# Kernel optimization log

Measured on AMD Instinct MI355X. Metric: run time of the kernel, lower is better.

## Reference

```python
import jax, jax.numpy as jnp
import numpy as np

N_ROIS = 8192
C, S = 256, 7
D = C * S * S  # 12544 flattened RoI feature dim
NUM_CLASSES = 31
DIMS = {"cls": NUM_CLASSES + 1, "reg": 4 * NUM_CLASSES, "face": 3, "colour": 7, "motion": 2}


def setup_inputs() -> dict:
    key = jax.random.key(0)
    ks = jax.random.split(key, 6)
    x = jax.random.normal(ks[0], (N_ROIS, C, S, S), dtype=jnp.float32)
    inp = {"x": x}
    for i, (name, out_dim) in enumerate(DIMS.items()):
        inp[f"W_{name}"] = 0.01 * jax.random.normal(ks[i + 1], (D, out_dim), dtype=jnp.float32)
        inp[f"b_{name}"] = jnp.zeros((out_dim,), dtype=jnp.float32)
    return inp


def reference(x, W_cls, b_cls, W_reg, b_reg, W_face, b_face,
              W_colour, b_colour, W_motion, b_motion):
    # AttributeBBoxHead.forward with with_avg_pool=False: flatten then 5 linear heads.
    xf = x.reshape(x.shape[0], -1)  # (N, 12544)
    cls_score = xf @ W_cls + b_cls        # (N, 32)
    bbox_pred = xf @ W_reg + b_reg        # (N, 124)
    face_score = xf @ W_face + b_face     # (N, 3)
    colour_score = xf @ W_colour + b_colour  # (N, 7)
    motion_score = xf @ W_motion + b_motion  # (N, 2)
    return (cls_score, bbox_pred, face_score, colour_score, motion_score)
```

## Files before the change

kernel.cpp:

```cpp
#include <hip/hip_runtime.h>
#include <hip/hip_bf16.h>
#include <stdint.h>

#define D_DIM 12544
#define NROIS 8192
#define NCOLS 168
#define NCPAD 176
#define NT 11
#define SPLIT 8
#define KSPLIT (D_DIM / SPLIT)
#define BK 32
#define KITERS (KSPLIT / BK)
#define BM 64

#define XROW_B 72
#define WCOL_B 80
#define WL_COLS 192
#define XL_BYTES (BM * XROW_B)
#define WL_BYTES (WL_COLS * WCOL_B)
#define BUF_BYTES (XL_BYTES + WL_BYTES)

typedef __attribute__((ext_vector_type(8))) short short8;
typedef __attribute__((ext_vector_type(4))) float floatx4;

__device__ __forceinline__ uint32_t pk_bf16(float a, float b) {
    uint32_t ua = __float_as_uint(a);
    uint32_t ub = __float_as_uint(b);
    ua = (ua + 0x7FFFu + ((ua >> 16) & 1u)) >> 16;
    ub = (ub + 0x7FFFu + ((ub >> 16) & 1u)) >> 16;
    return ua | (ub << 16);
}

__global__ __launch_bounds__(256) void pack_w(
        const float* __restrict__ Wc, const float* __restrict__ Wr,
        const float* __restrict__ Wf, const float* __restrict__ Wco,
        const float* __restrict__ Wm, uint16_t* __restrict__ Wp) {
    __shared__ float tile[64][33];
    int k0 = blockIdx.x * 64;
    int c0 = blockIdx.y * 32;
    int t  = threadIdx.x;

    int rc = t & 31;
    int rk = t >> 5;
#pragma unroll
    for (int rr = 0; rr < 8; ++rr) {
        int k = rr * 8 + rk;
        int kk = k0 + k;
        int c = c0 + rc;
        float v = 0.f;
        if (c < 32)       v = Wc[(size_t)kk * 32  + c];
        else if (c < 156) v = Wr[(size_t)kk * 124 + (c - 32)];
        else if (c < 159) v = Wf[(size_t)kk * 3   + (c - 156)];
        else if (c < 166) v = Wco[(size_t)kk * 7  + (c - 159)];
        else if (c < 168) v = Wm[(size_t)kk * 2   + (c - 166)];
        tile[k][rc] = v;
    }
    __syncthreads();

    int wc = t >> 3;
    int wk = t & 7;
    int c  = c0 + wc;
    if (c < NCPAD) {
        uint32_t o[4];
#pragma unroll
        for (int j = 0; j < 4; ++j)
            o[j] = pk_bf16(tile[wk * 8 + 2 * j][wc], tile[wk * 8 + 2 * j + 1][wc]);
        uint4 v = make_uint4(o[0], o[1], o[2], o[3]);
        *(uint4*)(Wp + (size_t)c * D_DIM + k0 + wk * 8) = v;
    }
}

__global__ __launch_bounds__(256) void gemm_split(const float* __restrict__ X,
                                                  const uint16_t* __restrict__ Wp,
                                                  uint16_t* __restrict__ parts) {
    __shared__ __attribute__((aligned(16))) char lds[2 * BUF_BYTES];

    int b     = blockIdx.x;
    int split = b & 7;
    int rb    = b >> 3;
    int row0  = rb * BM;
    int kbase = split * KSPLIT;

    int t    = threadIdx.x;
    int wave = t >> 6;
    int lane = t & 63;

    int sx_row = t >> 2;
    int sx_kc  = t & 3;
    const float* xg = X + (size_t)(row0 + sx_row) * D_DIM + kbase + sx_kc * 8;

    int sw_col = t >> 2;
    int sw_ch  = t & 3;
    int c0g = sw_col       < NCPAD ? sw_col       : NCPAD - 1;
    int c1g = sw_col + 64  < NCPAD ? sw_col + 64  : NCPAD - 1;
    int c2g = sw_col + 128 < NCPAD ? sw_col + 128 : NCPAD - 1;
    const uint16_t* wg0 = Wp + (size_t)c0g * D_DIM + kbase + sw_ch * 8;
    const uint16_t* wg1 = Wp + (size_t)c1g * D_DIM + kbase + sw_ch * 8;
    const uint16_t* wg2 = Wp + (size_t)c2g * D_DIM + kbase + sw_ch * 8;

    int x_st = sx_row * XROW_B + sx_kc * 16;
    int w_st0 = XL_BYTES + (sw_col)       * WCOL_B + sw_ch * 16;
    int w_st1 = XL_BYTES + (sw_col + 64)  * WCOL_B + sw_ch * 16;
    int w_st2 = XL_BYTES + (sw_col + 128) * WCOL_B + sw_ch * 16;

    int n    = lane & 15;
    int quad = lane >> 4;
    int xf_off = (wave * 16 + n) * XROW_B + quad * 16;
    int wf_off = XL_BYTES + n * WCOL_B + quad * 16;

    floatx4 acc[NT];
#pragma unroll
    for (int tt = 0; tt < NT; ++tt) acc[tt] = (floatx4)0.f;

    float4 px0 = *(const float4*)xg;
    float4 px1 = *(const float4*)(xg + 4);
    xg += BK;
    short8 pw0 = *(const short8*)wg0; wg0 += BK;
    short8 pw1 = *(const short8*)wg1; wg1 += BK;
    short8 pw2 = *(const short8*)wg2; wg2 += BK;
    {
        union { uint32_t u[4]; short8 s; } p;
        p.u[0] = pk_bf16(px0.x, px0.y); p.u[1] = pk_bf16(px0.z, px0.w);
        p.u[2] = pk_bf16(px1.x, px1.y); p.u[3] = pk_bf16(px1.z, px1.w);
        *(short8*)(lds + x_st) = p.s;
        *(short8*)(lds + w_st0) = pw0;
        *(short8*)(lds + w_st1) = pw1;
        *(short8*)(lds + w_st2) = pw2;
    }
    int cur = 0;

    for (int it = 0; it < KITERS; ++it) {
        __syncthreads();

        float4 nx0, nx1; short8 nw0, nw1, nw2;
        bool more = (it + 1 < KITERS);
        if (more) {
            nx0 = *(const float4*)xg;
            nx1 = *(const float4*)(xg + 4);
            xg += BK;
            nw0 = *(const short8*)wg0; wg0 += BK;
            nw1 = *(const short8*)wg1; wg1 += BK;
            nw2 = *(const short8*)wg2; wg2 += BK;
        }

        const char* cb = lds + cur * BUF_BYTES;
        short8 xf = *(const short8*)(cb + xf_off);
#pragma unroll
        for (int tt = 0; tt < NT; ++tt) {
            short8 wf = *(const short8*)(cb + wf_off + tt * (16 * WCOL_B));
            acc[tt] = __builtin_amdgcn_mfma_f32_16x16x32_bf16(wf, xf, acc[tt], 0, 0, 0);
        }

        if (more) {
            char* nb = lds + (cur ^ 1) * BUF_BYTES;
            union { uint32_t u[4]; short8 s; } p;
            p.u[0] = pk_bf16(nx0.x, nx0.y); p.u[1] = pk_bf16(nx0.z, nx0.w);
            p.u[2] = pk_bf16(nx1.x, nx1.y); p.u[3] = pk_bf16(nx1.z, nx1.w);
            *(short8*)(nb + x_st) = p.s;
            *(short8*)(nb + w_st0) = nw0;
            *(short8*)(nb + w_st1) = nw1;
            *(short8*)(nb + w_st2) = nw2;
            cur ^= 1;
        }
    }

    uint16_t* pb = parts + ((size_t)split * NROIS + row0 + wave * 16 + n) * NCOLS;
#pragma unroll
    for (int tt = 0; tt < NT; ++tt) {
        int col0 = tt * 16 + quad * 4;
        if (col0 + 3 < NCOLS) {
            uint32_t lo = pk_bf16(acc[tt].x, acc[tt].y);
            uint32_t hi = pk_bf16(acc[tt].z, acc[tt].w);
            uint2 v = make_uint2(lo, hi);
            *(uint2*)(pb + col0) = v;
        }
    }
}

__global__ void reduce_out(const uint16_t* __restrict__ parts,
                           const float* __restrict__ bc, const float* __restrict__ br,
                           const float* __restrict__ bf, const float* __restrict__ bco,
                           const float* __restrict__ bm, float* __restrict__ out) {
    int r = blockIdx.x;
    int c = threadIdx.x;
    if (c >= NCOLS) return;
    const size_t S = (size_t)NROIS * NCOLS;
    size_t off = (size_t)r * NCOLS + c;
    float v = 0.f;
#pragma unroll
    for (int s = 0; s < SPLIT; ++s)
        v += __uint_as_float((uint32_t)parts[off + (size_t)s * S] << 16);
    float bias; size_t oidx;
    if (c < 32)       { bias = bc[c];        oidx = (size_t)r * 32  + c; }
    else if (c < 156) { bias = br[c - 32];   oidx = 262144u  + (size_t)r * 124 + (c - 32); }
    else if (c < 159) { bias = bf[c - 156];  oidx = 1277952u + (size_t)r * 3   + (c - 156); }
    else if (c < 166) { bias = bco[c - 159]; oidx = 1302528u + (size_t)r * 7   + (c - 159); }
    else              { bias = bm[c - 166];  oidx = 1359872u + (size_t)r * 2   + (c - 166); }
    out[oidx] = v + bias;
}

extern "C" void kernel_launch(void* const* d_in, const int* in_sizes, int n_in,
                              void* d_out, int out_size, void* d_ws, size_t ws_size,
                              hipStream_t stream) {
    const float* X   = (const float*)d_in[0];
    const float* Wc  = (const float*)d_in[1];
    const float* bc  = (const float*)d_in[2];
    const float* Wr  = (const float*)d_in[3];
    const float* br  = (const float*)d_in[4];
    const float* Wf  = (const float*)d_in[5];
    const float* bfa = (const float*)d_in[6];
    const float* Wco = (const float*)d_in[7];
    const float* bco = (const float*)d_in[8];
    const float* Wm  = (const float*)d_in[9];
    const float* bm  = (const float*)d_in[10];

    uint16_t* Wp    = (uint16_t*)d_ws;
    uint16_t* parts = (uint16_t*)((char*)d_ws + (size_t)NCPAD * D_DIM * 2);
    float* out = (float*)d_out;

    pack_w<<<dim3(D_DIM / 64, 6), 256, 0, stream>>>(Wc, Wr, Wf, Wco, Wm, Wp);
    gemm_split<<<1024, 256, 0, stream>>>(X, Wp, parts);
    reduce_out<<<NROIS, 192, 0, stream>>>(parts, bc, br, bfa, bco, bm, out);
}
```

Before: 609.3 us.

## Deepen global prefetch to two stages with ping-pong registers in split GEMM

The K loop of the split-K GEMM now holds two sets of prefetch registers (A/B) and unrolls by two. Global loads are issued two iterations ahead instead of one, while LDS stays double-buffered. This gives more memory latency hiding for the streamed X reads. The launch bounds also now request 4 blocks per CU, which caps registers. The extra prefetch registers could cause spills or lower occupancy under that cap.

Result: no change. 620.0 us (+1.8%).

```diff
diff --git a/kernel.cpp b/kernel.cpp
--- a/kernel.cpp
+++ b/kernel.cpp
@@ -70,9 +70,9 @@
     }
 }
 
-__global__ __launch_bounds__(256) void gemm_split(const float* __restrict__ X,
-                                                  const uint16_t* __restrict__ Wp,
-                                                  uint16_t* __restrict__ parts) {
+__global__ __launch_bounds__(256, 4) void gemm_split(const float* __restrict__ X,
+                                                     const uint16_t* __restrict__ Wp,
+                                                     uint16_t* __restrict__ parts) {
     __shared__ __attribute__((aligned(16))) char lds[2 * BUF_BYTES];
 
     int b     = blockIdx.x;
@@ -98,7 +98,7 @@
     const uint16_t* wg1 = Wp + (size_t)c1g * D_DIM + kbase + sw_ch * 8;
     const uint16_t* wg2 = Wp + (size_t)c2g * D_DIM + kbase + sw_ch * 8;
 
-    int x_st = sx_row * XROW_B + sx_kc * 16;
+    int x_st  = sx_row * XROW_B + sx_kc * 16;
     int w_st0 = XL_BYTES + (sw_col)       * WCOL_B + sw_ch * 16;
     int w_st1 = XL_BYTES + (sw_col + 64)  * WCOL_B + sw_ch * 16;
     int w_st2 = XL_BYTES + (sw_col + 128) * WCOL_B + sw_ch * 16;
@@ -112,55 +112,63 @@
 #pragma unroll
     for (int tt = 0; tt < NT; ++tt) acc[tt] = (floatx4)0.f;
 
-    float4 px0 = *(const float4*)xg;
-    float4 px1 = *(const float4*)(xg + 4);
-    xg += BK;
-    short8 pw0 = *(const short8*)wg0; wg0 += BK;
-    short8 pw1 = *(const short8*)wg1; wg1 += BK;
-    short8 pw2 = *(const short8*)wg2; wg2 += BK;
-    {
+    float4 ax0, ax1; short8 aw0, aw1, aw2;
+    float4 bx0, bx1; short8 bw0, bw1, bw2;
+
+    auto issueA = [&]() {
+        ax0 = *(const float4*)xg; ax1 = *(const float4*)(xg + 4); xg += BK;
+        aw0 = *(const short8*)wg0; wg0 += BK;
+        aw1 = *(const short8*)wg1; wg1 += BK;
+        aw2 = *(const short8*)wg2; wg2 += BK;
+    };
+    auto issueB = [&]() {
+        bx0 = *(const float4*)xg; bx1 = *(const float4*)(xg + 4); xg += BK;
+        bw0 = *(const short8*)wg0; wg0 += BK;
+        bw1 = *(const short8*)wg1; wg1 += BK;
+        bw2 = *(const short8*)wg2; wg2 += BK;
+    };
+    auto stageA = [&](char* nb) {
         union { uint32_t u[4]; short8 s; } p;
-        p.u[0] = pk_bf16(px0.x, px0.y); p.u[1] = pk_bf16(px0.z, px0.w);
-        p.u[2] = pk_bf16(px1.x, px1.y); p.u[3] = pk_bf16(px1.z, px1.w);
-        *(short8*)(lds + x_st) = p.s;
-        *(short8*)(lds + w_st0) = pw0;
-        *(short8*)(lds + w_st1) = pw1;
-        *(short8*)(lds + w_st2) = pw2;
-    }
-    int cur = 0;
-
-    for (int it = 0; it < KITERS; ++it) {
-        __syncthreads();
-
-        float4 nx0, nx1; short8 nw0, nw1, nw2;
-        bool more = (it + 1 < KITERS);
-        if (more) {
-            nx0 = *(const float4*)xg;
-            nx1 = *(const float4*)(xg + 4);
-            xg += BK;
-            nw0 = *(const short8*)wg0; wg0 += BK;
-            nw1 = *(const short8*)wg1; wg1 += BK;
-            nw2 = *(const short8*)wg2; wg2 += BK;
-        }
-
-        const char* cb = lds + cur * BUF_BYTES;
+        p.u[0] = pk_bf16(ax0.x, ax0.y); p.u[1] = pk_bf16(ax0.z, ax0.w);
+        p.u[2] = pk_bf16(ax1.x, ax1.y); p.u[3] = pk_bf16(ax1.z, ax1.w);
+        *(short8*)(nb + x_st)  = p.s;
+        *(short8*)(nb + w_st0) = aw0;
+        *(short8*)(nb + w_st1) = aw1;
+        *(short8*)(nb + w_st2) = aw2;
+    };
+    auto stageB = [&](char* nb) {
+        union { uint32_t u[4]; short8 s; } p;
+        p.u[0] = pk_bf16(bx0.x, bx0.y); p.u[1] = pk_bf16(bx0.z, bx0.w);
+        p.u[2] = pk_bf16(bx1.x, bx1.y); p.u[3] = pk_bf16(bx1.z, bx1.w);
+        *(short8*)(nb + x_st)  = p.s;
+        *(short8*)(nb + w_st0) = bw0;
+        *(short8*)(nb + w_st1) = bw1;
+        *(short8*)(nb + w_st2) = bw2;
+    };
+    auto compute = [&](const char* cb) {
         short8 xf = *(const short8*)(cb + xf_off);
 #pragma unroll
         for (int tt = 0; tt < NT; ++tt) {
             short8 wf = *(const short8*)(cb + wf_off + tt * (16 * WCOL_B));
             acc[tt] = __builtin_amdgcn_mfma_f32_16x16x32_bf16(wf, xf, acc[tt], 0, 0, 0);
         }
-
-        if (more) {
-            char* nb = lds + (cur ^ 1) * BUF_BYTES;
-            union { uint32_t u[4]; short8 s; } p;
-            p.u[0] = pk_bf16(nx0.x, nx0.y); p.u[1] = pk_bf16(nx0.z, nx0.w);
-            p.u[2] = pk_bf16(nx1.x, nx1.y); p.u[3] = pk_bf16(nx1.z, nx1.w);
-            *(short8*)(nb + x_st) = p.s;
-            *(short8*)(nb + w_st0) = nw0;
-            *(short8*)(nb + w_st1) = nw1;
-            *(short8*)(nb + w_st2) = nw2;
-            cur ^= 1;
+    };
+
+    issueA();
+    issueB();
+    stageA(lds);
+
+    for (int it = 0; it < KITERS; it += 2) {
+        __syncthreads();
+        if (it + 2 < KITERS) issueA();
+        compute(lds);
+        if (it + 1 < KITERS) stageB(lds + BUF_BYTES);
+
+        __syncthreads();
+        if (it + 1 < KITERS) {
+            if (it + 3 < KITERS) issueB();
+            compute(lds + BUF_BYTES);
+            if (it + 2 < KITERS) stageA(lds);
         }
     }
 
```
